# Kernel tuning notes

Measured on AMD Instinct MI355X. Metric: run time of the kernel, lower is better.

Reference implementation:

```python
import jax, jax.numpy as jnp
import numpy as np

NQ, NK = 32, 128  # local window sizes from AttentionIndex defaults
N_HEADS = 8


def _build_index(M):
    """Precompute block-sparse local attention indices (static, numpy).
    Returns query_idx [C,NQ], query_mask [C,NQ], key_idx [C,NK], key_mask [C,NK].
    """
    C = (M + NQ - 1) // NQ
    half = (NQ - 1.0) * 0.5
    centers = np.round(np.arange(half, M + half, NQ, dtype=np.float32)).astype(np.int64)
    q_idx = np.arange(C * NQ, dtype=np.int64)
    q_mask = q_idx < M
    q_idx = np.where(q_mask, q_idx, 0).reshape(C, NQ)
    q_mask = q_mask.reshape(C, NQ)
    key_idx = np.zeros((C, NK), np.int64)
    key_mask = np.zeros((C, NK), bool)
    for i, c in enumerate(centers):
        s = max(int(c) - NK // 2, 0)
        e = min(int(c) + NK // 2, M)
        w = e - s
        key_idx[i, :w] = np.arange(s, e, dtype=np.int64)
        key_mask[i, :w] = True
    return (jnp.asarray(q_idx), jnp.asarray(q_mask),
            jnp.asarray(key_idx), jnp.asarray(key_mask))


def setup_inputs() -> dict:
    key = jax.random.key(0)
    ks = jax.random.split(key, 6)
    B, M, D, N = 2, 16384, 256, 2048
    f_atom = jax.random.normal(ks[0], (B, M, D), jnp.float32)
    atom_mask = jnp.ones((B, M), jnp.float32)
    atom_token_uid = jnp.sort(jax.random.randint(ks[1], (B, M), 0, N), axis=-1)
    scale = 1.0 / np.sqrt(D)
    Wq = jax.random.normal(ks[2], (D, D), jnp.float32) * scale
    Wk = jax.random.normal(ks[3], (D, D), jnp.float32) * scale
    Wv = jax.random.normal(ks[4], (D, D), jnp.float32) * scale
    Wo = jax.random.normal(ks[5], (D, D), jnp.float32) * scale
    return {"f_atom": f_atom, "atom_mask": atom_mask, "Wq": Wq, "Wk": Wk,
            "Wv": Wv, "Wo": Wo, "atom_token_uid": atom_token_uid, "n_token": N}


def reference(f_atom, atom_mask, Wq, Wk, Wv, Wo, atom_token_uid, n_token):
    B, M, D = f_atom.shape
    H = N_HEADS
    dh = D // H
    q_idx, q_mask, k_idx, k_mask = _build_index(M)
    C = q_idx.shape[0]

    # projections -> [B,M,H,dh]
    q = (f_atom @ Wq).reshape(B, M, H, dh)
    k = (f_atom @ Wk).reshape(B, M, H, dh)
    v = (f_atom @ Wv).reshape(B, M, H, dh)

    # gather into local windows: queries [B,C,NQ,H,dh], keys/values [B,C,NK,H,dh]
    qb = q[:, q_idx]
    kb = k[:, k_idx]
    vb = v[:, k_idx]

    key_valid = (atom_mask[:, k_idx] > 0) & k_mask[None]            # [B,C,NK]
    alpha_mask = q_mask[None, None, :, :, None] & key_valid[:, None, :, None, :]  # [B,H,C,NQ,NK] (bcast)

    scores = jnp.einsum('bcqhd,bckhd->bhcqk', qb, kb) / np.sqrt(dh)  # [B,H,C,NQ,NK]
    scores = jnp.where(alpha_mask, scores, jnp.float32(-1e9))
    attn = jax.nn.softmax(scores, axis=-1)

    out = jnp.einsum('bhcqk,bckhd->bcqhd', attn, vb)                 # [B,C,NQ,H,dh]
    out = out.reshape(B, C * NQ, D)[:, :M] @ Wo                      # scatter back to [B,M,D]
    out = out * atom_mask[..., None]

    # aggregate atom feats -> token feats (masked segment mean), pad to n_token
    def agg(data, seg, mask):
        s = jax.ops.segment_sum(data * mask[:, None], seg, num_segments=n_token)
        cnt = jax.ops.segment_sum(mask, seg, num_segments=n_token)
        return s / (cnt[:, None] + 1e-8)

    f_token = jax.vmap(agg)(out, atom_token_uid, atom_mask)          # [B,N,D]
    return f_token
```

## Files before the change

### kernel.cpp

```cpp
#include <hip/hip_runtime.h>

typedef _Float16 f16;
typedef _Float16 f16x4 __attribute__((ext_vector_type(4)));
typedef _Float16 f16x8 __attribute__((ext_vector_type(8)));
typedef float    f32x16 __attribute__((ext_vector_type(16)));

#define MFMA(a, b, c) __builtin_amdgcn_mfma_f32_32x32x16_f16((a), (b), (c), 0, 0, 0)

static constexpr int Mg   = 16384;
static constexpr int Bg   = 2;
static constexpr int Dg   = 256;
static constexpr int Hg   = 8;
static constexpr int Cg   = 512;
static constexpr int Ntok = 2048;
static constexpr float QSCALE = 0.25503487f;

typedef __attribute__((address_space(1))) const void gbl_cv;
typedef __attribute__((address_space(3))) void lds_v;

static __device__ __forceinline__ void gll16(const f16* g, f16* l) {
    __builtin_amdgcn_global_load_lds((gbl_cv*)g, (lds_v*)l, 16, 0, 0);
}
static __device__ __forceinline__ f16x8 mk8(f16x4 a, f16x4 b) {
    f16x8 r;
    r[0] = a[0]; r[1] = a[1]; r[2] = a[2]; r[3] = a[3];
    r[4] = b[0]; r[5] = b[1]; r[6] = b[2]; r[7] = b[3];
    return r;
}

__global__ __launch_bounds__(256) void k_wt(const float* __restrict__ Wq,
                                            const float* __restrict__ Wk,
                                            const float* __restrict__ Wv,
                                            const float* __restrict__ Wo,
                                            const int* __restrict__ uid,
                                            f16* __restrict__ Wsw,
                                            int* __restrict__ starts) {
    int idx = blockIdx.x * 256 + threadIdx.x;
    int w   = idx >> 16;
    int rem = idx & 65535;
    int k   = rem >> 8;
    int n   = rem & 255;
    if (w < 3) {
        const float* W = (w == 0) ? Wq : (w == 1) ? Wk : Wv;
        int G = (k >> 3) ^ (n & 7);
        Wsw[w * 65536 + n * 256 + (G << 3) + (k & 7)] = (f16)W[k * 256 + n];
    } else {
        Wsw[3 * 65536 + ((k >> 3) * 256 + n) * 8 + (k & 7)] = (f16)Wo[k * 256 + n];
    }
    if (idx < 2 * 2049) {
        int b = idx / 2049, t = idx % 2049;
        const int* u = uid + b * Mg;
        int lo = 0, hi = Mg;
        while (lo < hi) { int mid = (lo + hi) >> 1; if (u[mid] < t) lo = mid + 1; else hi = mid; }
        starts[idx] = lo;
    }
}

__global__ __launch_bounds__(256, 2) void k_qkv(const float* __restrict__ A,
                                                const f16* __restrict__ Wsw,
                                                f16* __restrict__ Qo,
                                                f16* __restrict__ Ko,
                                                f16* __restrict__ VW) {
    __shared__ f16 Ls[2][32 * 256];

    const int tid  = threadIdx.x;
    const int d    = blockIdx.x;
    const int lin  = (d & 7) * 64 + (d >> 3);
    const int yt   = lin >> 1;
    const int half = lin & 1;
    const int m0   = yt * 128;
    const int lane = tid & 63, w = tid >> 6;
    const int l31  = lane & 31, hi = lane >> 5;
    const int mrow = m0 + 32 * w + l31;
    const int xr   = l31 & 7;

#define STW(S, BB)                                                             \
    {                                                                          \
        const f16* src = Wsw + ((S) >> 3) * 65536 + (((S) & 7) * 32) * 256;    \
        _Pragma("unroll")                                                      \
        for (int i = 0; i < 4; ++i) {                                          \
            int g2 = i * 256 + tid;                                            \
            gll16(src + g2 * 8, &Ls[BB][g2 * 8]);                              \
        }                                                                      \
    }

    if (half == 0) { STW(0, 0); } else { STW(12, 0); }

    f16x8 a[16];
    const float* ap = A + (size_t)mrow * 256 + 8 * hi;
#pragma unroll
    for (int g = 0; g < 16; ++g) {
        float4 v0 = *reinterpret_cast<const float4*>(ap + 16 * g);
        float4 v1 = *reinterpret_cast<const float4*>(ap + 16 * g + 4);
        f16x8 t;
        t[0] = (f16)v0.x; t[1] = (f16)v0.y; t[2] = (f16)v0.z; t[3] = (f16)v0.w;
        t[4] = (f16)v1.x; t[5] = (f16)v1.y; t[6] = (f16)v1.z; t[7] = (f16)v1.w;
        a[g] = t;
    }

#define QKV_STEP(S, BB)                                                        \
    {                                                                          \
        if ((S) + 1 < s_end) { STW((S) + 1, (BB) ^ 1); }                       \
        f32x16 acc;                                                            \
        _Pragma("unroll")                                                      \
        for (int e = 0; e < 16; ++e) acc[e] = 0.f;                             \
        _Pragma("unroll")                                                      \
        for (int g = 0; g < 16; ++g) {                                         \
            f16x8 bf = *(const f16x8*)&Ls[BB][l31 * 256 +                      \
                                             (((2 * g + hi) ^ xr) << 3)];      \
            acc = MFMA(a[g], bf, acc);                                         \
        }                                                                      \
        const int wix  = (S) >> 3;                                             \
        const int gcol = ((S) & 7) * 32 + l31;                                 \
        const int mb   = m0 + 32 * w + 4 * hi;                                 \
        if (wix == 0) {                                                        \
            _Pragma("unroll")                                                  \
            for (int r = 0; r < 16; ++r)                                       \
                Qo[(size_t)(mb + (r & 3) + 8 * (r >> 2)) * 256 + gcol] =       \
                    (f16)(acc[r] * QSCALE);                                    \
        } else if (wix == 1) {                                                 \
            _Pragma("unroll")                                                  \
            for (int r = 0; r < 16; ++r)                                       \
                Ko[(size_t)(mb + (r & 3) + 8 * (r >> 2)) * 256 + gcol] =       \
                    (f16)acc[r];                                               \
        } else {                                                               \
            _Pragma("unroll")                                                  \
            for (int rq = 0; rq < 4; ++rq) {                                   \
                f16x4 pv = { (f16)acc[rq * 4 + 0], (f16)acc[rq * 4 + 1],       \
                             (f16)acc[rq * 4 + 2], (f16)acc[rq * 4 + 3] };     \
                int mr  = mb + 8 * rq;                                         \
                int bb2 = mr >> 14;                                            \
                int msg = (mr & 16383) >> 3;                                   \
                *reinterpret_cast<f16x4*>(VW + ((size_t)(bb2 * 2048 + msg) *   \
                                          256 + gcol) * 8 + 4 * hi) = pv;      \
            }                                                                  \
        }                                                                      \
        if ((S) + 1 < s_end) {                                                 \
            if (((S) >> 3) == 2) {                                             \
                asm volatile("s_waitcnt vmcnt(4)" ::: "memory");               \
            } else {                                                           \
                asm volatile("s_waitcnt vmcnt(16)" ::: "memory");              \
            }                                                                  \
            __builtin_amdgcn_s_barrier();                                      \
            __builtin_amdgcn_sched_barrier(0);                                 \
        }                                                                      \
    }

#define QKV_RUN(BASE)                                                          \
    {                                                                          \
        const int s_end = (BASE) + 12;                                         \
        asm volatile("s_waitcnt vmcnt(0)" ::: "memory");                       \
        __builtin_amdgcn_s_barrier();                                          \
        __builtin_amdgcn_sched_barrier(0);                                     \
        _Pragma("unroll")                                                      \
        for (int ss = 0; ss < 12; ++ss) { QKV_STEP((BASE) + ss, ss & 1); }     \
    }

    if (half == 0) { QKV_RUN(0); } else { QKV_RUN(12); }
#undef QKV_RUN
#undef QKV_STEP
#undef STW
}

__global__ __launch_bounds__(512, 2) void k_attn(const f16* __restrict__ Qo,
                                                 const f16* __restrict__ Ko,
                                                 const f16* __restrict__ VW,
                                                 const f16* __restrict__ Wsw,
                                                 f16* __restrict__ OUT) {
    __shared__ f16 Ks[128 * 256];
    __shared__ f16 Qs[32 * 256];

    const int tid  = threadIdx.x;
    const int idx  = blockIdx.x;
    const int lin  = (idx & 7) * 128 + (idx >> 3);
    const int b    = lin >> 9;
    const int c    = lin & 511;
    const int h    = tid >> 6;
    const int l31  = tid & 31;
    const int hi   = (tid & 63) >> 5;

    const int u0 = 32 * c - 48;
    const int e0 = (32 * c + 80 < Mg) ? (32 * c + 80) : Mg;
    const bool full = (u0 >= 0) && (32 * c + 80 <= Mg);

    const f16* Kb = Ko + (size_t)b * Mg * 256;
#pragma unroll
    for (int i = 0; i < 8; ++i) {
        int g = i * 512 + tid;
        int r = g >> 5, s = g & 31;
        int m = u0 + r;
        m = m < 0 ? 0 : (m > Mg - 1 ? Mg - 1 : m);
        gll16(Kb + (size_t)m * 256 + ((s ^ (r & 31)) << 3), &Ks[g * 8]);
    }
    const f16* Qb = Qo + ((size_t)b * Mg + 32 * c) * 256;
#pragma unroll
    for (int i = 0; i < 2; ++i) {
        int g = i * 512 + tid;
        int r = g >> 5, s = g & 31;
        gll16(Qb + (size_t)r * 256 + ((s ^ r) << 3), &Qs[g * 8]);
    }
    __syncthreads();

    const f16* Vbb = VW + (size_t)b * 2048 * 256 * 8;
    f16x4 v0r[8], v1r[8];
#pragma unroll
    for (int s = 0; s < 8; ++s) {
        int g0 = (u0 >> 3) + 2 * s;
        int g1 = g0 + 1;
        g0 = g0 < 0 ? 0 : (g0 > 2047 ? 2047 : g0);
        g1 = g1 < 0 ? 0 : (g1 > 2047 ? 2047 : g1);
        v0r[s] = *(const f16x4*)(Vbb + ((size_t)g0 * 256 + 32 * h + l31) * 8 + 4 * hi);
        v1r[s] = *(const f16x4*)(Vbb + ((size_t)g1 * 256 + 32 * h + l31) * 8 + 4 * hi);
    }

    f16x8 qf0 = *(const f16x8*)&Qs[l31 * 256 + (((4 * h + hi) ^ l31) << 3)];
    f16x8 qf1 = *(const f16x8*)&Qs[l31 * 256 + (((4 * h + 2 + hi) ^ l31) << 3)];

    f32x16 p4[4];
#pragma unroll
    for (int t = 0; t < 4; ++t)
#pragma unroll
        for (int e = 0; e < 16; ++e) p4[t][e] = 0.f;

    __builtin_amdgcn_s_setprio(1);
#pragma unroll
    for (int t = 0; t < 4; ++t) {
        int rr = 32 * t + l31;
        f16x8 kf0 = *(const f16x8*)&Ks[rr * 256 + (((4 * h + hi) ^ l31) << 3)];
        f16x8 kf1 = *(const f16x8*)&Ks[rr * 256 + (((4 * h + 2 + hi) ^ l31) << 3)];
        p4[t] = MFMA(kf0, qf0, p4[t]);
        p4[t] = MFMA(kf1, qf1, p4[t]);
    }
    __builtin_amdgcn_s_setprio(0);

    float mx = -3e38f;
    float sum = 0.f;
    if (full) {
#pragma unroll
        for (int t = 0; t < 4; ++t)
#pragma unroll
            for (int r = 0; r < 16; ++r) mx = fmaxf(mx, p4[t][r]);
        mx = fmaxf(mx, __shfl_xor(mx, 32));
#pragma unroll
        for (int t = 0; t < 4; ++t)
#pragma unroll
            for (int r = 0; r < 16; ++r) {
                float ev = exp2f(p4[t][r] - mx);
                p4[t][r] = ev;
                sum += ev;
            }
    } else {
#pragma unroll
        for (int t = 0; t < 4; ++t)
#pragma unroll
            for (int r = 0; r < 16; ++r) {
                int gm = u0 + 32 * t + (r & 3) + 8 * (r >> 2) + 4 * hi;
                if (gm >= 0 && gm < e0) mx = fmaxf(mx, p4[t][r]);
            }
        mx = fmaxf(mx, __shfl_xor(mx, 32));
#pragma unroll
        for (int t = 0; t < 4; ++t)
#pragma unroll
            for (int r = 0; r < 16; ++r) {
                int gm = u0 + 32 * t + (r & 3) + 8 * (r >> 2) + 4 * hi;
                float ev = (gm >= 0 && gm < e0) ? exp2f(p4[t][r] - mx) : 0.f;
                p4[t][r] = ev;
                sum += ev;
            }
    }
    sum += __shfl_xor(sum, 32);
    const float inv = 1.f / sum;
#pragma unroll
    for (int t = 0; t < 4; ++t)
#pragma unroll
        for (int e = 0; e < 16; ++e) p4[t][e] *= inv;

    asm volatile("s_waitcnt vmcnt(0)" ::: "memory");
    __builtin_amdgcn_sched_barrier(0);

    f32x16 o;
#pragma unroll
    for (int e = 0; e < 16; ++e) o[e] = 0.f;

    __builtin_amdgcn_s_setprio(1);
#pragma unroll
    for (int s = 0; s < 8; ++s) {
        f16x8 pa;
#pragma unroll
        for (int e = 0; e < 8; ++e) pa[e] = (f16)(p4[s >> 1][8 * (s & 1) + e]);
        o = MFMA(pa, mk8(v0r[s], v1r[s]), o);
    }
    __builtin_amdgcn_s_setprio(0);

    __syncthreads();
    {
        const int col = h * 32 + l31;
#pragma unroll
        for (int r = 0; r < 16; ++r) {
            int row = (r & 3) + 8 * (r >> 2) + 4 * hi;
            Ks[row * 264 + col] = (f16)o[r];
        }
    }
    __syncthreads();

    {
        const f16* Wb = Wsw + 3 * 65536;
        f32x16 acc;
#pragma unroll
        for (int e = 0; e < 16; ++e) acc[e] = 0.f;
        __builtin_amdgcn_s_setprio(1);
#pragma unroll
        for (int g = 0; g < 16; ++g) {
            int gp = 2 * g + hi;
            f16x8 av = *(const f16x8*)&Ks[l31 * 264 + gp * 8];
            f16x8 bv = *(const f16x8*)(Wb + ((size_t)gp * 256 + 32 * h + l31) * 8);
            acc = MFMA(av, bv, acc);
        }
        __builtin_amdgcn_s_setprio(0);
#pragma unroll
        for (int r = 0; r < 16; ++r) {
            int row = (r & 3) + 8 * (r >> 2) + 4 * hi;
            OUT[((size_t)b * Mg + 32 * c + row) * 256 + h * 32 + l31] = (f16)acc[r];
        }
    }
}

__global__ __launch_bounds__(256) void k_seg(const f16* __restrict__ OUT,
                                             const int* __restrict__ starts,
                                             const float* __restrict__ mask,
                                             float* __restrict__ out) {
    const int t = blockIdx.x, b = blockIdx.y;
    const int d = threadIdx.x;

    const int lo  = starts[b * 2049 + t];
    const int lo2 = starts[b * 2049 + t + 1];

    float sum = 0.f, cnt = 0.f;
    for (int m = lo; m < lo2; ++m) {
        float msk = mask[b * Mg + m];
        sum += msk * msk * (float)OUT[((size_t)b * Mg + m) * 256 + d];
        cnt += msk;
    }
    out[((size_t)b * Ntok + t) * 256 + d] = sum / (cnt + 1e-8f);
}

extern "C" void kernel_launch(void* const* d_in, const int* in_sizes, int n_in,
                              void* d_out, int out_size, void* d_ws, size_t ws_size,
                              hipStream_t stream) {
    const float* f_atom = (const float*)d_in[0];
    const float* amask  = (const float*)d_in[1];
    const float* Wq     = (const float*)d_in[2];
    const float* Wk     = (const float*)d_in[3];
    const float* Wv     = (const float*)d_in[4];
    const float* Wo     = (const float*)d_in[5];
    const int*   uid    = (const int*)d_in[6];

    const size_t HALF_WT  = 4 * 65536;
    const size_t HALF_MAT = (size_t)Bg * Mg * Dg;
    const size_t needed_bytes = (HALF_WT + 4 * HALF_MAT) * sizeof(f16) + 2 * 2049 * sizeof(int);
    if (ws_size < needed_bytes) return;

    f16* Wsw  = (f16*)d_ws;
    f16* Qb   = Wsw + HALF_WT;
    f16* Kb   = Qb + HALF_MAT;
    f16* VWb  = Kb + HALF_MAT;
    f16* OUTb = VWb + HALF_MAT;
    int* starts = (int*)(OUTb + HALF_MAT);

    k_wt  <<<dim3(1024), 256, 0, stream>>>(Wq, Wk, Wv, Wo, uid, Wsw, starts);
    k_qkv <<<dim3(512), 256, 0, stream>>>(f_atom, Wsw, Qb, Kb, VWb);
    k_attn<<<dim3(1024), 512, 0, stream>>>(Qb, Kb, VWb, Wsw, OUTb);
    k_seg <<<dim3(Ntok, Bg), 256, 0, stream>>>(OUTb, starts, amask, (float*)d_out);
}
```

Measured before the change: 76.88 us.

## Fuse segment-mean aggregation into attention epilogue via atomics

Removes the separate segment-mean kernel and the f16 intermediate output buffer. The setup kernel now precomputes a per-token inverse count. The attention kernel scales each atom's output-projection result by mask² times that inverse and atomically adds it into the zeroed token output. This saves a full write and read of the per-atom output and one launch. In exchange it adds a memset and many fp32 atomics, which contend when several atoms map to the same token, and the order of float summation becomes nondeterministic.

```diff
diff --git a/kernel.cpp b/kernel.cpp
--- a/kernel.cpp
+++ b/kernel.cpp
@@ -33,8 +33,9 @@
                                             const float* __restrict__ Wv,
                                             const float* __restrict__ Wo,
                                             const int* __restrict__ uid,
+                                            const float* __restrict__ mask,
                                             f16* __restrict__ Wsw,
-                                            int* __restrict__ starts) {
+                                            float* __restrict__ inv) {
     int idx = blockIdx.x * 256 + threadIdx.x;
     int w   = idx >> 16;
     int rem = idx & 65535;
@@ -47,12 +48,16 @@
     } else {
         Wsw[3 * 65536 + ((k >> 3) * 256 + n) * 8 + (k & 7)] = (f16)Wo[k * 256 + n];
     }
-    if (idx < 2 * 2049) {
-        int b = idx / 2049, t = idx % 2049;
+    if (idx < 2 * 2048) {
+        int b = idx >> 11, t = idx & 2047;
         const int* u = uid + b * Mg;
         int lo = 0, hi = Mg;
         while (lo < hi) { int mid = (lo + hi) >> 1; if (u[mid] < t) lo = mid + 1; else hi = mid; }
-        starts[idx] = lo;
+        int lo2 = lo, hi2 = Mg;
+        while (lo2 < hi2) { int mid = (lo2 + hi2) >> 1; if (u[mid] < t + 1) lo2 = mid + 1; else hi2 = mid; }
+        float cnt = 0.f;
+        for (int m = lo; m < lo2; ++m) cnt += mask[b * Mg + m];
+        inv[idx] = 1.f / (cnt + 1e-8f);
     }
 }
 
@@ -166,7 +171,10 @@
                                                  const f16* __restrict__ Ko,
                                                  const f16* __restrict__ VW,
                                                  const f16* __restrict__ Wsw,
-                                                 f16* __restrict__ OUT) {
+                                                 const int* __restrict__ uid,
+                                                 const float* __restrict__ mask,
+                                                 const float* __restrict__ inv,
+                                                 float* __restrict__ fout) {
     __shared__ f16 Ks[128 * 256];
     __shared__ f16 Qs[32 * 256];
 
@@ -269,11 +277,11 @@
             }
     }
     sum += __shfl_xor(sum, 32);
-    const float inv = 1.f / sum;
+    const float invs = 1.f / sum;
 #pragma unroll
     for (int t = 0; t < 4; ++t)
 #pragma unroll
-        for (int e = 0; e < 16; ++e) p4[t][e] *= inv;
+        for (int e = 0; e < 16; ++e) p4[t][e] *= invs;
 
     asm volatile("s_waitcnt vmcnt(0)" ::: "memory");
     __builtin_amdgcn_sched_barrier(0);
@@ -300,6 +308,13 @@
             int row = (r & 3) + 8 * (r >> 2) + 4 * hi;
             Ks[row * 264 + col] = (f16)o[r];
         }
+    }
+    if (tid < 32) {
+        int m = 32 * c + tid;
+        int t = uid[b * Mg + m];
+        float msk = mask[b * Mg + m];
+        *reinterpret_cast<float*>(&Qs[2 * tid])      = msk * msk * inv[b * 2048 + t];
+        *reinterpret_cast<int*>(&Qs[64 + 2 * tid])   = t;
     }
     __syncthreads();
 
@@ -320,28 +335,11 @@
 #pragma unroll
         for (int r = 0; r < 16; ++r) {
             int row = (r & 3) + 8 * (r >> 2) + 4 * hi;
-            OUT[((size_t)b * Mg + 32 * c + row) * 256 + h * 32 + l31] = (f16)acc[r];
+            float s = *reinterpret_cast<const float*>(&Qs[2 * row]);
+            int   t = *reinterpret_cast<const int*>(&Qs[64 + 2 * row]);
+            atomicAdd(&fout[((size_t)b * Ntok + t) * 256 + h * 32 + l31], acc[r] * s);
         }
     }
-}
-
-__global__ __launch_bounds__(256) void k_seg(const f16* __restrict__ OUT,
-                                             const int* __restrict__ starts,
-                                             const float* __restrict__ mask,
-                                             float* __restrict__ out) {
-    const int t = blockIdx.x, b = blockIdx.y;
-    const int d = threadIdx.x;
-
-    const int lo  = starts[b * 2049 + t];
-    const int lo2 = starts[b * 2049 + t + 1];
-
-    float sum = 0.f, cnt = 0.f;
-    for (int m = lo; m < lo2; ++m) {
-        float msk = mask[b * Mg + m];
-        sum += msk * msk * (float)OUT[((size_t)b * Mg + m) * 256 + d];
-        cnt += msk;
-    }
-    out[((size_t)b * Ntok + t) * 256 + d] = sum / (cnt + 1e-8f);
 }
 
 extern "C" void kernel_launch(void* const* d_in, const int* in_sizes, int n_in,
@@ -357,18 +355,19 @@
 
     const size_t HALF_WT  = 4 * 65536;
     const size_t HALF_MAT = (size_t)Bg * Mg * Dg;
-    const size_t needed_bytes = (HALF_WT + 4 * HALF_MAT) * sizeof(f16) + 2 * 2049 * sizeof(int);
+    const size_t needed_bytes = (HALF_WT + 3 * HALF_MAT) * sizeof(f16) + 2 * 2048 * sizeof(float);
     if (ws_size < needed_bytes) return;
 
     f16* Wsw  = (f16*)d_ws;
     f16* Qb   = Wsw + HALF_WT;
     f16* Kb   = Qb + HALF_MAT;
     f16* VWb  = Kb + HALF_MAT;
-    f16* OUTb = VWb + HALF_MAT;
-    int* starts = (int*)(OUTb + HALF_MAT);
-
-    k_wt  <<<dim3(1024), 256, 0, stream>>>(Wq, Wk, Wv, Wo, uid, Wsw, starts);
+    float* inv = (float*)(VWb + HALF_MAT);
+
+    hipMemsetAsync(d_out, 0, (size_t)out_size * sizeof(float), stream);
+
+    k_wt  <<<dim3(1024), 256, 0, stream>>>(Wq, Wk, Wv, Wo, uid, amask, Wsw, inv);
     k_qkv <<<dim3(512), 256, 0, stream>>>(f_atom, Wsw, Qb, Kb, VWb);
-    k_attn<<<dim3(1024), 512, 0, stream>>>(Qb, Kb, VWb, Wsw, OUTb);
-    k_seg <<<dim3(Ntok, Bg), 256, 0, stream>>>(OUTb, starts, amask, (float*)d_out);
-}
+    k_attn<<<dim3(1024), 512, 0, stream>>>(Qb, Kb, VWb, Wsw, uid, amask, inv,
+                                           (float*)d_out);
+}
```

New measurement: 117.3 us. 52.5% more time.
